# Kernel tuning notes

Measured on AMD Instinct MI355X. Metric: run time of the kernel, lower is better.

Reference implementation:

```python
import jax, jax.numpy as jnp
import numpy as np

N, IN, OUT, RANK = 8192, 4096, 4096, 16
SCALING = 2.0

def setup_inputs() -> dict:
    key = jax.random.key(0)
    k1, k2, k3, k4 = jax.random.split(key, 4)
    x = jax.random.normal(k1, (N, IN), dtype=jnp.float32)
    weight = jax.random.normal(k2, (OUT, IN), dtype=jnp.float32) * (1.0 / np.sqrt(IN))
    lora_A = jax.random.normal(k3, (RANK, IN), dtype=jnp.float32) * (1.0 / np.sqrt(IN))
    lora_B = jax.random.normal(k4, (OUT, RANK), dtype=jnp.float32) * 0.01
    return {"x": x, "weight": weight, "lora_A": lora_A, "lora_B": lora_B}

def reference(x, weight, lora_A, lora_B):
    # frozen base linear: F.linear(x, weight) == x @ weight.T  -> [N, OUT]
    base = jnp.einsum('ni,oi->no', x, weight)
    # LoRA branch: dropout(x) (p=0 => identity) @ A.T @ B.T, scaled
    lora = jnp.einsum('ni,ri->nr', x, lora_A)      # [N, RANK]
    lora = jnp.einsum('nr,or->no', lora, lora_B)   # [N, OUT]
    return base + lora * SCALING
```

## Files before the change

kernel.cpp:

```cpp
#include <hip/hip_runtime.h>


#define N_ROWS 8192
#define K_DIM  4096
#define N_COLS 4096
#define RANK   16
#define BK     64
#define NT     (K_DIM / BK)

typedef __bf16 bf16x8 __attribute__((ext_vector_type(8)));
typedef float  f32x4  __attribute__((ext_vector_type(4)));

__device__ __forceinline__ unsigned short f2bf(float f) {
  unsigned int u = __builtin_bit_cast(unsigned int, f);
  u += 0x7FFFu + ((u >> 16) & 1u);
  return (unsigned short)(u >> 16);
}


__global__ __launch_bounds__(256) void conv_x_kernel(const float* __restrict__ x,
                                                     unsigned short* __restrict__ xb) {
  size_t idx = (size_t)blockIdx.x * blockDim.x + threadIdx.x;
  const float4 v = *reinterpret_cast<const float4*>(x + idx * 4);
  ushort4 r;
  r.x = f2bf(v.x); r.y = f2bf(v.y); r.z = f2bf(v.z); r.w = f2bf(v.w);
  *reinterpret_cast<ushort4*>(xb + idx * 4) = r;
}

__global__ __launch_bounds__(256) void make_weff_kernel(const float* __restrict__ w,
                                                        const float* __restrict__ A,
                                                        const float* __restrict__ Bm,
                                                        unsigned short* __restrict__ wb) {
  size_t idx = (size_t)blockIdx.x * blockDim.x + threadIdx.x;
  int o  = (int)(idx >> 10);
  int ic = (int)(idx & 1023) << 2;
  const float4 wv = *reinterpret_cast<const float4*>(w + (size_t)o * K_DIM + ic);
  float a0 = wv.x, a1 = wv.y, a2 = wv.z, a3 = wv.w;
  float br[RANK];
#pragma unroll
  for (int r4 = 0; r4 < RANK / 4; ++r4) {
    const float4 bv = *reinterpret_cast<const float4*>(Bm + (size_t)o * RANK + r4 * 4);
    br[r4 * 4 + 0] = bv.x; br[r4 * 4 + 1] = bv.y;
    br[r4 * 4 + 2] = bv.z; br[r4 * 4 + 3] = bv.w;
  }
#pragma unroll
  for (int r = 0; r < RANK; ++r) {
    const float4 av = *reinterpret_cast<const float4*>(A + (size_t)r * K_DIM + ic);
    float b2 = br[r] * 2.0f;
    a0 += b2 * av.x; a1 += b2 * av.y; a2 += b2 * av.z; a3 += b2 * av.w;
  }
  ushort4 rr;
  rr.x = f2bf(a0); rr.y = f2bf(a1); rr.z = f2bf(a2); rr.w = f2bf(a3);
  *reinterpret_cast<ushort4*>(wb + (size_t)o * K_DIM + ic) = rr;
}


__device__ __forceinline__ void gload_lds16(const void* g, void* l) {
  __builtin_amdgcn_global_load_lds(
      (__attribute__((address_space(1))) void*)g,
      (__attribute__((address_space(3))) void*)l, 16, 0, 0);
}

__global__ __launch_bounds__(512, 1) void gemm_bf16_look(
    const unsigned short* __restrict__ xb, const unsigned short* __restrict__ wb,
    float* __restrict__ out) {
  __shared__ __align__(16) char smem[131072];

  const int t  = threadIdx.x;
  const int l  = t & 63;
  const int wv = t >> 6;
  const int lr = l & 15;
  const int lk = l >> 4;
  const int wr = wv >> 2;
  const int wc = wv & 3;

  const int bid  = blockIdx.x;
  const int sbid = (bid & 7) * 64 + (bid >> 3);
  const int bm   = sbid >> 4;
  const int bn   = sbid & 15;

  const int srow = t >> 3;
  const int scol = ((t & 7) ^ ((t >> 3) & 7)) << 3;
  const unsigned short* gA = xb + (size_t)(bm * 256 + srow) * K_DIM + scol;
  const unsigned short* gB = wb + (size_t)(bn * 256 + srow) * K_DIM + scol;
  char* ldsA = smem + t * 16;
  char* ldsB = smem + 65536 + t * 16;

#define STG_A(hh, SRC, NB) do {                                                 \
    const unsigned short* _g = (SRC) + (size_t)((hh) * 128) * K_DIM;            \
    char* _l = ldsA + (NB) + (hh) * 16384;                                      \
    gload_lds16(_g, _l);                                                        \
    gload_lds16(_g + (size_t)64 * K_DIM, _l + 8192);                            \
  } while (0)
#define STG_B(hh, SRC, NB) do {                                                 \
    const unsigned short* _g = (SRC) + (size_t)((hh) * 128) * K_DIM;            \
    char* _l = ldsB + (NB) + (hh) * 16384;                                      \
    gload_lds16(_g, _l);                                                        \
    gload_lds16(_g + (size_t)64 * K_DIM, _l + 8192);                            \
  } while (0)

  const int g0   = (lk ^ (lr & 7)) << 4;
  const int g1   = ((lk + 4) ^ (lr & 7)) << 4;
  const int aoff = (wr * 16 + lr) * 128;
  const int boff = (wc * 16 + lr) * 128;

  bf16x8 aE[8], aO[8], bO[4], bE[2][4];
  f32x4 acc[8][4];
#pragma unroll
  for (int m = 0; m < 8; ++m)
#pragma unroll
    for (int n = 0; n < 4; ++n)
      acc[m][n] = (f32x4){0.f, 0.f, 0.f, 0.f};

#define RD_A(DST, BASE) do {                                                    \
    _Pragma("unroll")                                                           \
    for (int m = 0; m < 4; ++m) {                                               \
      DST[2 * m + 0] = *(const bf16x8*)(smem + (BASE) + m * 4096 + aoff + g0);  \
      DST[2 * m + 1] = *(const bf16x8*)(smem + (BASE) + m * 4096 + aoff + g1);  \
    }                                                                           \
  } while (0)
#define RD_B(DST, BASE) do {                                                    \
    _Pragma("unroll")                                                           \
    for (int n = 0; n < 2; ++n) {                                               \
      DST[2 * n + 0] = *(const bf16x8*)(smem + 65536 + (BASE) + n * 8192 + boff + g0); \
      DST[2 * n + 1] = *(const bf16x8*)(smem + 65536 + (BASE) + n * 8192 + boff + g1); \
    }                                                                           \
  } while (0)

#define MFMA_Q(MB, AF, NB0, BF) do {                                            \
    _Pragma("unroll")                                                           \
    for (int mi = 0; mi < 4; ++mi)                                              \
      _Pragma("unroll")                                                         \
      for (int ni = 0; ni < 2; ++ni)                                            \
        _Pragma("unroll")                                                       \
        for (int kk = 0; kk < 2; ++kk)                                          \
          acc[(MB) + mi][(NB0) + ni] = __builtin_amdgcn_mfma_f32_16x16x32_bf16( \
              AF[mi * 2 + kk], BF[ni * 2 + kk], acc[(MB) + mi][(NB0) + ni], 0, 0, 0); \
  } while (0)

#define PH_END(VM) do {                                                         \
    __builtin_amdgcn_sched_barrier(0);                                          \
    asm volatile("s_waitcnt vmcnt(" #VM ")");                                   \
    __builtin_amdgcn_s_barrier();                                               \
    __builtin_amdgcn_sched_barrier(0);                                          \
  } while (0)

#define TILE(CB, NB, PC, PN, T) do {                                            \
    const int _tk = ((T) + 1 < NT) ? (T) + 1 : NT - 1;                          \
    const unsigned short* _sA = gA + (size_t)_tk * BK;                          \
    const unsigned short* _sB = gB + (size_t)_tk * BK;                          \
                     \
    RD_B(bO, (CB) + 16384);                                                     \
    STG_A(0, _sA, NB); STG_B(0, _sB, NB); STG_B(1, _sB, NB);                    \
    __builtin_amdgcn_sched_barrier(0);                                          \
    __builtin_amdgcn_s_setprio(1); MFMA_Q(0, aE, 0, bE[PC]);                    \
    __builtin_amdgcn_s_setprio(0);                                              \
    PH_END(6);                                                                  \
                               \
    RD_A(aO, (CB) + 16384);                                                     \
    STG_A(1, _sA, NB);                                                          \
    __builtin_amdgcn_sched_barrier(0);                                          \
    __builtin_amdgcn_s_setprio(1); MFMA_Q(0, aE, 2, bO);                        \
    __builtin_amdgcn_s_setprio(0);                                              \
    PH_END(6);                                                                  \
                                            \
    RD_A(aE, (NB));                                                             \
    __builtin_amdgcn_sched_barrier(0);                                          \
    __builtin_amdgcn_s_setprio(1); MFMA_Q(4, aO, 2, bO);                        \
    __builtin_amdgcn_s_setprio(0);                                              \
    PH_END(4);                                                                  \
                                    \
    RD_B(bE[PN], (NB));                                                         \
    __builtin_amdgcn_sched_barrier(0);                                          \
    __builtin_amdgcn_s_setprio(1); MFMA_Q(4, aO, 0, bE[PC]);                    \
    __builtin_amdgcn_s_setprio(0);                                              \
    PH_END(2);                                                                  \
  } while (0)

  STG_A(0, gA, 0); STG_A(1, gA, 0); STG_B(0, gB, 0); STG_B(1, gB, 0);
  __builtin_amdgcn_sched_barrier(0);
  asm volatile("s_waitcnt vmcnt(0)");
  __builtin_amdgcn_s_barrier();
  __builtin_amdgcn_sched_barrier(0);
  RD_A(aE, 0);
  RD_B(bE[0], 0);

#pragma nounroll
  for (int u = 0; u < NT / 2; ++u) {
    TILE(0, 32768, 0, 1, 2 * u);
    TILE(32768, 0, 1, 0, 2 * u + 1);
  }

  asm volatile("s_waitcnt vmcnt(0)");

  const int orow = bm * 256 + wr * 16 + lk * 4;
  const int ocol = bn * 256 + wc * 16 + lr;
#pragma unroll
  for (int mf = 0; mf < 8; ++mf)
#pragma unroll
    for (int nf = 0; nf < 4; ++nf)
#pragma unroll
      for (int j = 0; j < 4; ++j)
        out[(size_t)(orow + mf * 32 + j) * N_COLS + (ocol + nf * 64)] = acc[mf][nf][j];

#undef STG_A
#undef STG_B
#undef RD_A
#undef RD_B
#undef MFMA_Q
#undef PH_END
#undef TILE
}


__global__ __launch_bounds__(256) void fallback_kernel(const float* __restrict__ x,
                                                       const float* __restrict__ w,
                                                       const float* __restrict__ A,
                                                       const float* __restrict__ Bm,
                                                       float* __restrict__ out) {
  const int o    = blockIdx.x * 256 + threadIdx.x;
  const int nrow = blockIdx.y;
  float bro[RANK];
#pragma unroll
  for (int r = 0; r < RANK; ++r) bro[r] = Bm[(size_t)o * RANK + r] * 2.0f;
  float bacc = 0.f;
  float tacc[RANK];
#pragma unroll
  for (int r = 0; r < RANK; ++r) tacc[r] = 0.f;
  for (int k = 0; k < K_DIM; ++k) {
    float xv = x[(size_t)nrow * K_DIM + k];
    bacc += xv * w[(size_t)o * K_DIM + k];
#pragma unroll
    for (int r = 0; r < RANK; ++r) tacc[r] += xv * A[(size_t)r * K_DIM + k];
  }
  float res = bacc;
#pragma unroll
  for (int r = 0; r < RANK; ++r) res += bro[r] * tacc[r];
  out[(size_t)nrow * N_COLS + o] = res;
}


extern "C" void kernel_launch(void* const* d_in, const int* in_sizes, int n_in,
                              void* d_out, int out_size, void* d_ws, size_t ws_size,
                              hipStream_t stream) {
  const float* x  = (const float*)d_in[0];
  const float* w  = (const float*)d_in[1];
  const float* A  = (const float*)d_in[2];
  const float* Bm = (const float*)d_in[3];
  float* out = (float*)d_out;

  const size_t need = ((size_t)N_ROWS * K_DIM + (size_t)N_COLS * K_DIM) * sizeof(unsigned short);
  if (ws_size < need) {
    dim3 grid(N_COLS / 256, N_ROWS);
    fallback_kernel<<<grid, 256, 0, stream>>>(x, w, A, Bm, out);
    return;
  }

  unsigned short* xb = (unsigned short*)d_ws;
  unsigned short* wb = xb + (size_t)N_ROWS * K_DIM;

  conv_x_kernel<<<(N_ROWS * K_DIM / 4) / 256, 256, 0, stream>>>(x, xb);
  make_weff_kernel<<<(N_COLS * K_DIM / 4) / 256, 256, 0, stream>>>(w, A, Bm, wb);

  const int grid_gemm = (N_ROWS / 256) * (N_COLS / 256);
  gemm_bf16_look<<<grid_gemm, 512, 0, stream>>>(xb, wb, out);
}
```

Measured before the change: 349.9 us.

## Merge prep kernels and restructure GEMM pipeline with deeper prefetch and fewer fragment registers

```diff
diff --git a/kernel.cpp b/kernel.cpp
--- a/kernel.cpp
+++ b/kernel.cpp
@@ -8,6 +8,9 @@
 #define BK     64
 #define NT     (K_DIM / BK)
 
+#define XBLK ((N_ROWS * K_DIM / 4) / 256)
+#define WBLK ((N_COLS * K_DIM / 4) / 256)
+
 typedef __bf16 bf16x8 __attribute__((ext_vector_type(8)));
 typedef float  f32x4  __attribute__((ext_vector_type(4)));
 
@@ -18,40 +21,42 @@
 }
 
 
-__global__ __launch_bounds__(256) void conv_x_kernel(const float* __restrict__ x,
-                                                     unsigned short* __restrict__ xb) {
-  size_t idx = (size_t)blockIdx.x * blockDim.x + threadIdx.x;
-  const float4 v = *reinterpret_cast<const float4*>(x + idx * 4);
-  ushort4 r;
-  r.x = f2bf(v.x); r.y = f2bf(v.y); r.z = f2bf(v.z); r.w = f2bf(v.w);
-  *reinterpret_cast<ushort4*>(xb + idx * 4) = r;
-}
-
-__global__ __launch_bounds__(256) void make_weff_kernel(const float* __restrict__ w,
-                                                        const float* __restrict__ A,
-                                                        const float* __restrict__ Bm,
-                                                        unsigned short* __restrict__ wb) {
-  size_t idx = (size_t)blockIdx.x * blockDim.x + threadIdx.x;
-  int o  = (int)(idx >> 10);
-  int ic = (int)(idx & 1023) << 2;
-  const float4 wv = *reinterpret_cast<const float4*>(w + (size_t)o * K_DIM + ic);
-  float a0 = wv.x, a1 = wv.y, a2 = wv.z, a3 = wv.w;
-  float br[RANK];
-#pragma unroll
-  for (int r4 = 0; r4 < RANK / 4; ++r4) {
-    const float4 bv = *reinterpret_cast<const float4*>(Bm + (size_t)o * RANK + r4 * 4);
-    br[r4 * 4 + 0] = bv.x; br[r4 * 4 + 1] = bv.y;
-    br[r4 * 4 + 2] = bv.z; br[r4 * 4 + 3] = bv.w;
-  }
-#pragma unroll
-  for (int r = 0; r < RANK; ++r) {
-    const float4 av = *reinterpret_cast<const float4*>(A + (size_t)r * K_DIM + ic);
-    float b2 = br[r] * 2.0f;
-    a0 += b2 * av.x; a1 += b2 * av.y; a2 += b2 * av.z; a3 += b2 * av.w;
-  }
-  ushort4 rr;
-  rr.x = f2bf(a0); rr.y = f2bf(a1); rr.z = f2bf(a2); rr.w = f2bf(a3);
-  *reinterpret_cast<ushort4*>(wb + (size_t)o * K_DIM + ic) = rr;
+__global__ __launch_bounds__(256) void prep_kernel(const float* __restrict__ x,
+                                                   const float* __restrict__ w,
+                                                   const float* __restrict__ A,
+                                                   const float* __restrict__ Bm,
+                                                   unsigned short* __restrict__ xb,
+                                                   unsigned short* __restrict__ wb) {
+  const int b = blockIdx.x;
+  if (b < XBLK) {
+    size_t idx = (size_t)b * 256 + threadIdx.x;
+    const float4 v = *reinterpret_cast<const float4*>(x + idx * 4);
+    ushort4 r;
+    r.x = f2bf(v.x); r.y = f2bf(v.y); r.z = f2bf(v.z); r.w = f2bf(v.w);
+    *reinterpret_cast<ushort4*>(xb + idx * 4) = r;
+  } else {
+    size_t idx = (size_t)(b - XBLK) * 256 + threadIdx.x;
+    int o  = (int)(idx >> 10);
+    int ic = (int)(idx & 1023) << 2;
+    const float4 wv = *reinterpret_cast<const float4*>(w + (size_t)o * K_DIM + ic);
+    float a0 = wv.x, a1 = wv.y, a2 = wv.z, a3 = wv.w;
+    float br[RANK];
+#pragma unroll
+    for (int r4 = 0; r4 < RANK / 4; ++r4) {
+      const float4 bv = *reinterpret_cast<const float4*>(Bm + (size_t)o * RANK + r4 * 4);
+      br[r4 * 4 + 0] = bv.x; br[r4 * 4 + 1] = bv.y;
+      br[r4 * 4 + 2] = bv.z; br[r4 * 4 + 3] = bv.w;
+    }
+#pragma unroll
+    for (int r = 0; r < RANK; ++r) {
+      const float4 av = *reinterpret_cast<const float4*>(A + (size_t)r * K_DIM + ic);
+      float b2 = br[r] * 2.0f;
+      a0 += b2 * av.x; a1 += b2 * av.y; a2 += b2 * av.z; a3 += b2 * av.w;
+    }
+    ushort4 rr;
+    rr.x = f2bf(a0); rr.y = f2bf(a1); rr.z = f2bf(a2); rr.w = f2bf(a3);
+    *reinterpret_cast<ushort4*>(wb + (size_t)o * K_DIM + ic) = rr;
+  }
 }
 
 
@@ -61,7 +66,7 @@
       (__attribute__((address_space(3))) void*)l, 16, 0, 0);
 }
 
-__global__ __launch_bounds__(512, 1) void gemm_bf16_look(
+__global__ __launch_bounds__(512, 1) void gemm_bf16_r7(
     const unsigned short* __restrict__ xb, const unsigned short* __restrict__ wb,
     float* __restrict__ out) {
   __shared__ __align__(16) char smem[131072];
@@ -104,7 +109,9 @@
   const int aoff = (wr * 16 + lr) * 128;
   const int boff = (wc * 16 + lr) * 128;
 
-  bf16x8 aE[8], aO[8], bO[4], bE[2][4];
+  bf16x8 aF[8];
+  bf16x8 bE[4];
+  bf16x8 bO[4];
   f32x4 acc[8][4];
 #pragma unroll
   for (int m = 0; m < 8; ++m)
@@ -112,11 +119,11 @@
     for (int n = 0; n < 4; ++n)
       acc[m][n] = (f32x4){0.f, 0.f, 0.f, 0.f};
 
-#define RD_A(DST, BASE) do {                                                    \
+#define RD_A(BASE) do {                                                         \
     _Pragma("unroll")                                                           \
     for (int m = 0; m < 4; ++m) {                                               \
-      DST[2 * m + 0] = *(const bf16x8*)(smem + (BASE) + m * 4096 + aoff + g0);  \
-      DST[2 * m + 1] = *(const bf16x8*)(smem + (BASE) + m * 4096 + aoff + g1);  \
+      aF[2 * m + 0] = *(const bf16x8*)(smem + (BASE) + m * 4096 + aoff + g0);   \
+      aF[2 * m + 1] = *(const bf16x8*)(smem + (BASE) + m * 4096 + aoff + g1);   \
     }                                                                           \
   } while (0)
 #define RD_B(DST, BASE) do {                                                    \
@@ -127,7 +134,7 @@
     }                                                                           \
   } while (0)
 
-#define MFMA_Q(MB, AF, NB0, BF) do {                                            \
+#define MFMA_Q(MB, NB0, BF) do {                                                \
     _Pragma("unroll")                                                           \
     for (int mi = 0; mi < 4; ++mi)                                              \
       _Pragma("unroll")                                                         \
@@ -135,63 +142,78 @@
         _Pragma("unroll")                                                       \
         for (int kk = 0; kk < 2; ++kk)                                          \
           acc[(MB) + mi][(NB0) + ni] = __builtin_amdgcn_mfma_f32_16x16x32_bf16( \
-              AF[mi * 2 + kk], BF[ni * 2 + kk], acc[(MB) + mi][(NB0) + ni], 0, 0, 0); \
-  } while (0)
-
-#define PH_END(VM) do {                                                         \
-    __builtin_amdgcn_sched_barrier(0);                                          \
-    asm volatile("s_waitcnt vmcnt(" #VM ")");                                   \
-    __builtin_amdgcn_s_barrier();                                               \
-    __builtin_amdgcn_sched_barrier(0);                                          \
-  } while (0)
-
-#define TILE(CB, NB, PC, PN, T) do {                                            \
-    const int _tk = ((T) + 1 < NT) ? (T) + 1 : NT - 1;                          \
-    const unsigned short* _sA = gA + (size_t)_tk * BK;                          \
-    const unsigned short* _sB = gB + (size_t)_tk * BK;                          \
-                     \
+              aF[mi * 2 + kk], BF[ni * 2 + kk], acc[(MB) + mi][(NB0) + ni], 0, 0, 0); \
+  } while (0)
+
+#define PRE_LG() do {                                                           \
+    __builtin_amdgcn_sched_barrier(0);                                          \
+    __builtin_amdgcn_s_barrier();                                               \
+    asm volatile("s_waitcnt lgkmcnt(0)");                                       \
+    __builtin_amdgcn_sched_barrier(0);                                          \
+    __builtin_amdgcn_s_setprio(1);                                              \
+  } while (0)
+#define PRE_NOLG() do {                                                         \
+    __builtin_amdgcn_sched_barrier(0);                                          \
+    __builtin_amdgcn_s_barrier();                                               \
+    __builtin_amdgcn_sched_barrier(0);                                          \
+    __builtin_amdgcn_s_setprio(1);                                              \
+  } while (0)
+#define POST() do {                                                             \
+    __builtin_amdgcn_s_setprio(0);                                              \
+    __builtin_amdgcn_sched_barrier(0);                                          \
+    __builtin_amdgcn_s_barrier();                                               \
+    __builtin_amdgcn_sched_barrier(0);                                          \
+  } while (0)
+#define POST_VM4() do {                                                         \
+    __builtin_amdgcn_s_setprio(0);                                              \
+    __builtin_amdgcn_sched_barrier(0);                                          \
+    asm volatile("s_waitcnt vmcnt(4)");                                         \
+    __builtin_amdgcn_s_barrier();                                               \
+    __builtin_amdgcn_sched_barrier(0);                                          \
+  } while (0)
+
+#define TILE(CB, NB, T) do {                                                    \
+    const int _t1 = ((T) + 1 < NT) ? (T) + 1 : NT - 1;                          \
+    const int _t2 = ((T) + 2 < NT) ? (T) + 2 : NT - 1;                          \
+    const unsigned short* _sA1 = gA + (size_t)_t1 * BK;                         \
+    const unsigned short* _sB1 = gB + (size_t)_t1 * BK;                         \
+    const unsigned short* _sA2 = gA + (size_t)_t2 * BK;                         \
+    const unsigned short* _sB2 = gB + (size_t)_t2 * BK;                         \
+                    \
+    STG_A(1, _sA1, NB);                                                         \
+    RD_A((CB)); RD_B(bE, (CB));                                                 \
+    asm volatile("s_waitcnt lgkmcnt(8)");                                       \
+    PRE_LG(); MFMA_Q(0, 0, bE); POST();                                         \
+                       \
+    STG_B(0, _sB1, NB);                                                         \
     RD_B(bO, (CB) + 16384);                                                     \
-    STG_A(0, _sA, NB); STG_B(0, _sB, NB); STG_B(1, _sB, NB);                    \
-    __builtin_amdgcn_sched_barrier(0);                                          \
-    __builtin_amdgcn_s_setprio(1); MFMA_Q(0, aE, 0, bE[PC]);                    \
-    __builtin_amdgcn_s_setprio(0);                                              \
-    PH_END(6);                                                                  \
-                               \
-    RD_A(aO, (CB) + 16384);                                                     \
-    STG_A(1, _sA, NB);                                                          \
-    __builtin_amdgcn_sched_barrier(0);                                          \
-    __builtin_amdgcn_s_setprio(1); MFMA_Q(0, aE, 2, bO);                        \
-    __builtin_amdgcn_s_setprio(0);                                              \
-    PH_END(6);                                                                  \
-                                            \
-    RD_A(aE, (NB));                                                             \
-    __builtin_amdgcn_sched_barrier(0);                                          \
-    __builtin_amdgcn_s_setprio(1); MFMA_Q(4, aO, 2, bO);                        \
-    __builtin_amdgcn_s_setprio(0);                                              \
-    PH_END(4);                                                                  \
-                                    \
-    RD_B(bE[PN], (NB));                                                         \
-    __builtin_amdgcn_sched_barrier(0);                                          \
-    __builtin_amdgcn_s_setprio(1); MFMA_Q(4, aO, 0, bE[PC]);                    \
-    __builtin_amdgcn_s_setprio(0);                                              \
-    PH_END(2);                                                                  \
+    PRE_LG(); MFMA_Q(0, 2, bO); POST();                                         \
+                       \
+    STG_A(0, _sA2, CB);                                                         \
+    RD_A((CB) + 16384);                                                         \
+    PRE_LG(); MFMA_Q(4, 2, bO); POST();                                         \
+         \
+    STG_B(1, _sB2, CB);                                                         \
+    PRE_NOLG(); MFMA_Q(4, 0, bE); POST_VM4();                                   \
   } while (0)
 
   STG_A(0, gA, 0); STG_A(1, gA, 0); STG_B(0, gB, 0); STG_B(1, gB, 0);
+  {
+    const unsigned short* _pA1 = gA + (size_t)BK;
+    const unsigned short* _pB1 = gB + (size_t)BK;
+    STG_A(0, _pA1, 32768);
+    STG_B(1, _pB1, 32768);
+  }
   __builtin_amdgcn_sched_barrier(0);
-  asm volatile("s_waitcnt vmcnt(0)");
+  asm volatile("s_waitcnt vmcnt(4)");
   __builtin_amdgcn_s_barrier();
   __builtin_amdgcn_sched_barrier(0);
-  RD_A(aE, 0);
-  RD_B(bE[0], 0);
 
 #pragma nounroll
   for (int u = 0; u < NT / 2; ++u) {
-    TILE(0, 32768, 0, 1, 2 * u);
-    TILE(32768, 0, 1, 0, 2 * u + 1);
-  }
-
-  asm volatile("s_waitcnt vmcnt(0)");
+    TILE(0, 32768, 2 * u);
+    TILE(32768, 0, 2 * u + 1);
+  }
 
   const int orow = bm * 256 + wr * 16 + lk * 4;
   const int ocol = bn * 256 + wc * 16 + lr;
@@ -208,7 +230,10 @@
 #undef RD_A
 #undef RD_B
 #undef MFMA_Q
-#undef PH_END
+#undef PRE_LG
+#undef PRE_NOLG
+#undef POST
+#undef POST_VM4
 #undef TILE
 }
 
@@ -259,9 +284,8 @@
   unsigned short* xb = (unsigned short*)d_ws;
   unsigned short* wb = xb + (size_t)N_ROWS * K_DIM;
 
-  conv_x_kernel<<<(N_ROWS * K_DIM / 4) / 256, 256, 0, stream>>>(x, xb);
-  make_weff_kernel<<<(N_COLS * K_DIM / 4) / 256, 256, 0, stream>>>(w, A, Bm, wb);
+  prep_kernel<<<XBLK + WBLK, 256, 0, stream>>>(x, w, A, Bm, xb, wb);
 
   const int grid_gemm = (N_ROWS / 256) * (N_COLS / 256);
-  gemm_bf16_look<<<grid_gemm, 512, 0, stream>>>(xb, wb, out);
-}
+  gemm_bf16_r7<<<grid_gemm, 512, 0, stream>>>(xb, wb, out);
+}
```

New measurement: 314.1 us. -10.2%, faster.
